# Performance work log

Hardware: AMD Instinct MI355X
Metric: run time of the kernel (lower is better)

## Reference

```python
import jax, jax.numpy as jnp
import numpy as np

# Fixed directional 3x3 stencils (order j=0..3 as in the torch module)
_K0 = [[0, 0, 0], [-0.5, 1, -0.5], [0, 0, 0]]
_K1 = [[0, 0, -0.5], [0, 1, 0], [-0.5, 0, 0]]
_K2 = [[0, -0.5, 0], [0, 1, 0], [0, -0.5, 0]]
_K3 = [[-0.5, 0, 0], [0, 1, 0], [0, 0, -0.5]]
KERNELS = jnp.asarray(np.stack([_K0, _K1, _K2, _K3])[:, None], dtype=jnp.float32)  # [4,1,3,3] OIHW
_EPS = 1e-5


def setup_inputs() -> dict:
    key = jax.random.key(0)
    x = jax.random.normal(key, (32, 3, 512, 512), dtype=jnp.float32)
    return {"x": x}


def reference(x):
    # grayscale: [B,1,H,W]
    gray = (0.3 * x[:, 0] + 0.59 * x[:, 1] + 0.11 * x[:, 2])[:, None]
    # one conv with 4 output channels instead of 4 separate 1-channel convs
    ltpe = jax.lax.conv_general_dilated(
        gray, KERNELS, window_strides=(1, 1), padding=((1, 1), (1, 1)),
        dimension_numbers=("NCHW", "OIHW", "NCHW"))  # [B,4,H,W]
    coeffs = (2.0 ** jnp.arange(4, dtype=jnp.float32)) / 15.0  # 2^j / 15
    # sum_j ((ltpe_j + 1) * 0.5) * coeff_j  -> [B,1,H,W]
    out = jnp.einsum("bjhw,j->bhw", (ltpe + 1.0) * 0.5, coeffs)[:, None]
    # InstanceNorm2d(1): per-(batch, channel) normalization over H,W, biased var, no affine
    mean = jnp.mean(out, axis=(2, 3), keepdims=True)
    var = jnp.var(out, axis=(2, 3), keepdims=True)
    out = (out - mean) * jax.lax.rsqrt(var + _EPS)
    return jnp.concatenate([out, out, out], axis=1)  # [B,3,H,W]
```

## Files before the change

kernel.cpp:

```cpp
#include <hip/hip_runtime.h>
#include <hip/hip_fp16.h>

#define IMGS 32
#define H 512
#define W 512
#define NPIX (H * W)
#define NTHR 256
#define RB 8
#define NBANDS (H / RB)
#define C4W (W / 4)

__device__ __forceinline__ float sten(float C, float L, float R, float U, float D,
                                      float UL, float UR, float DL, float DR) {
    const float c0 = 1.0f / 15.0f, c1 = 2.0f / 15.0f;
    const float c2 = 4.0f / 15.0f, c3 = 8.0f / 15.0f;
    const float acc = c0 * (L + R) + c1 * (UR + DL) + c2 * (U + D) + c3 * (UL + DR);
    return fmaf(-0.25f, acc, fmaf(0.5f, C, 0.5f));
}

template <typename ST>
__global__ __launch_bounds__(NTHR, 6) void k1_stencil(
    const float* __restrict__ x, ST* sout, size_t sstride,
    float2* __restrict__ partials)
{
    __shared__ float G[RB + 2][W];

    const int tid  = threadIdx.x;
    const int blk  = blockIdx.x;
    const int img  = blk >> 6;
    const int band = blk & (NBANDS - 1);
    const int r0   = band * RB;

    const float* xbase = x + (size_t)img * 3 * NPIX;
    ST* sbase = sout + (size_t)img * sstride;

#pragma unroll
    for (int it = 0; it < (RB + 2) * C4W / NTHR; ++it) {
        const int idx = it * NTHR + tid;
        const int ri  = idx >> 7;
        const int c4  = idx & (C4W - 1);
        const int gr  = r0 - 1 + ri;
        float4 g4 = make_float4(0.f, 0.f, 0.f, 0.f);
        if ((unsigned)gr < (unsigned)H) {
            const float* p = xbase + gr * W + c4 * 4;
            const float4 r = *(const float4*)p;
            const float4 g = *(const float4*)(p + NPIX);
            const float4 b = *(const float4*)(p + 2 * NPIX);
            g4.x = fmaf(0.3f, r.x, fmaf(0.59f, g.x, 0.11f * b.x));
            g4.y = fmaf(0.3f, r.y, fmaf(0.59f, g.y, 0.11f * b.y));
            g4.z = fmaf(0.3f, r.z, fmaf(0.59f, g.z, 0.11f * b.z));
            g4.w = fmaf(0.3f, r.w, fmaf(0.59f, g.w, 0.11f * b.w));
        }
        *(float4*)&G[ri][c4 * 4] = g4;
    }
    __syncthreads();

    const int c4   = tid & (C4W - 1);
    const int half = tid >> 7;
    const int lr0  = half * (RB / 2);

    float sum = 0.0f, sq = 0.0f;

    float4 a4 = *(const float4*)&G[lr0][c4 * 4];
    float4 b4 = *(const float4*)&G[lr0 + 1][c4 * 4];
    float aL = (c4 == 0) ? 0.0f : G[lr0][c4 * 4 - 1];
    float aR = (c4 == C4W - 1) ? 0.0f : G[lr0][c4 * 4 + 4];
    float bL = (c4 == 0) ? 0.0f : G[lr0 + 1][c4 * 4 - 1];
    float bR = (c4 == C4W - 1) ? 0.0f : G[lr0 + 1][c4 * 4 + 4];

#pragma unroll
    for (int k = 0; k < RB / 2; ++k) {
        const int lr = lr0 + k + 2;
        const float4 d4 = *(const float4*)&G[lr][c4 * 4];
        const float dL = (c4 == 0) ? 0.0f : G[lr][c4 * 4 - 1];
        const float dR = (c4 == C4W - 1) ? 0.0f : G[lr][c4 * 4 + 4];

        float4 o;
        o.x = sten(b4.x, bL,   b4.y, a4.x, d4.x, aL,   a4.y, dL,   d4.y);
        o.y = sten(b4.y, b4.x, b4.z, a4.y, d4.y, a4.x, a4.z, d4.x, d4.z);
        o.z = sten(b4.z, b4.y, b4.w, a4.z, d4.z, a4.y, a4.w, d4.y, d4.w);
        o.w = sten(b4.w, b4.z, bR,   a4.w, d4.w, a4.z, aR,   d4.z, dR);

        sum += (o.x + o.y) + (o.z + o.w);
        sq = fmaf(o.x, o.x, sq); sq = fmaf(o.y, o.y, sq);
        sq = fmaf(o.z, o.z, sq); sq = fmaf(o.w, o.w, sq);

        const size_t off = (size_t)(r0 + half * (RB / 2) + k) * W + c4 * 4;
        if constexpr (sizeof(ST) == 2) {
            union { __half h[4]; float2 f; } u;
            u.h[0] = __float2half_rn(o.x);
            u.h[1] = __float2half_rn(o.y);
            u.h[2] = __float2half_rn(o.z);
            u.h[3] = __float2half_rn(o.w);
            *(float2*)(sbase + off) = u.f;
        } else {
            *(float4*)(sbase + off) = o;
        }

        a4 = b4; aL = bL; aR = bR;
        b4 = d4; bL = dL; bR = dR;
    }

#pragma unroll
    for (int off = 32; off > 0; off >>= 1) {
        sum += __shfl_down(sum, off);
        sq  += __shfl_down(sq, off);
    }
    __syncthreads();
    const int wave = tid >> 6;
    const int lane = tid & 63;
    if (lane == 0) { G[0][wave] = sum; G[0][4 + wave] = sq; }
    __syncthreads();
    if (tid == 0) {
        partials[blk] = make_float2((G[0][0] + G[0][1]) + (G[0][2] + G[0][3]),
                                    (G[0][4] + G[0][5]) + (G[0][6] + G[0][7]));
    }
}

template <typename ST>
__global__ __launch_bounds__(NTHR) void k2_norm(
    const float2* __restrict__ partials, const ST* sin, size_t sstride,
    float* __restrict__ out)
{
    __shared__ float sm[2];

    const int tid = threadIdx.x;
    const int blk = blockIdx.x;
    const int img = blk >> 8;
    const int bi  = blk & 255;

    if (tid < 64) {
        const float2 p = partials[img * NBANDS + tid];
        float S1 = p.x, S2 = p.y;
#pragma unroll
        for (int off = 32; off > 0; off >>= 1) {
            S1 += __shfl_down(S1, off);
            S2 += __shfl_down(S2, off);
        }
        if (tid == 0) {
            const float m = S1 * (1.0f / NPIX);
            const float v = S2 * (1.0f / NPIX) - m * m;
            sm[0] = m;
            sm[1] = rsqrtf(v + 1e-5f);
        }
    }
    __syncthreads();
    const float mean = sm[0];
    const float rstd = sm[1];

    const ST* sb = sin + (size_t)img * sstride;
    float* base = out + (size_t)img * 3 * NPIX;
    const size_t off = (size_t)(bi * NTHR + tid) * 4;

    float4 v;
    if constexpr (sizeof(ST) == 2) {
        union { float2 f; __half h[4]; } u;
        u.f = *(const float2*)(sb + off);
        v.x = __half2float(u.h[0]); v.y = __half2float(u.h[1]);
        v.z = __half2float(u.h[2]); v.w = __half2float(u.h[3]);
    } else {
        v = *(const float4*)(sb + off);
    }
    v.x = (v.x - mean) * rstd;
    v.y = (v.y - mean) * rstd;
    v.z = (v.z - mean) * rstd;
    v.w = (v.w - mean) * rstd;
    *(float4*)(base + off) = v;
    *(float4*)(base + NPIX + off) = v;
    *(float4*)(base + 2 * NPIX + off) = v;
}

extern "C" void kernel_launch(void* const* d_in, const int* in_sizes, int n_in,
                              void* d_out, int out_size, void* d_ws, size_t ws_size,
                              hipStream_t stream) {
    const float* x = (const float*)d_in[0];
    float* out = (float*)d_out;

    const size_t s_bytes = (size_t)IMGS * NPIX * sizeof(__half);
    const size_t need = s_bytes + (size_t)IMGS * NBANDS * sizeof(float2);

    if (ws_size >= need) {
        __half* s = (__half*)d_ws;
        float2* partials = (float2*)((char*)d_ws + s_bytes);
        k1_stencil<__half><<<dim3(IMGS * NBANDS), dim3(NTHR), 0, stream>>>(
            x, s, (size_t)NPIX, partials);
        k2_norm<__half><<<dim3(IMGS * 256), dim3(NTHR), 0, stream>>>(
            partials, s, (size_t)NPIX, out);
    } else {
        float2* partials = (float2*)d_ws;
        k1_stencil<float><<<dim3(IMGS * NBANDS), dim3(NTHR), 0, stream>>>(
            x, out, (size_t)(3 * NPIX), partials);
        k2_norm<float><<<dim3(IMGS * 256), dim3(NTHR), 0, stream>>>(
            partials, out, (size_t)(3 * NPIX), out);
    }
}
```

Baseline: 45.75 us.

## Fuse stencil and instance norm into one pass with cross-block stat handoff

Merges the two kernels into a single launch. Each block keeps its stencil outputs in registers, publishes per-band partial sums, and the last block per image (found via an atomic counter) computes mean and rstd; every block spins until those stats are published and then writes the normalized output directly. This removes the intermediate half-precision buffer write and read and one kernel launch, and doubles rows per band to 16 so there are 1024 blocks. It depends on all 1024 blocks being co-resident, since blocks spin-wait on others; launch bounds allow 4 blocks per CU, and a memset is added each call.

```diff
diff --git a/kernel.cpp b/kernel.cpp
--- a/kernel.cpp
+++ b/kernel.cpp
@@ -1,14 +1,14 @@
 #include <hip/hip_runtime.h>
-#include <hip/hip_fp16.h>
 
 #define IMGS 32
 #define H 512
 #define W 512
 #define NPIX (H * W)
 #define NTHR 256
-#define RB 8
+#define RB 16
 #define NBANDS (H / RB)
 #define C4W (W / 4)
+#define NBLK (IMGS * NBANDS)
 
 __device__ __forceinline__ float sten(float C, float L, float R, float U, float D,
                                       float UL, float UR, float DL, float DR) {
@@ -18,21 +18,26 @@
     return fmaf(-0.25f, acc, fmaf(0.5f, C, 0.5f));
 }
 
-template <typename ST>
-__global__ __launch_bounds__(NTHR, 6) void k1_stencil(
-    const float* __restrict__ x, ST* sout, size_t sstride,
-    float2* __restrict__ partials)
+union PackF2 { float2 f; unsigned long long u; };
+
+__global__ __launch_bounds__(NTHR, 4) void ltpe_onepass(
+    const float* __restrict__ x, float* __restrict__ out,
+    unsigned long long* __restrict__ stats,
+    int* __restrict__ counters,
+    unsigned long long* __restrict__ partials)
 {
     __shared__ float G[RB + 2][W];
+    __shared__ float red[8];
+    __shared__ int fin;
+    __shared__ float sstat[2];
 
     const int tid  = threadIdx.x;
     const int blk  = blockIdx.x;
-    const int img  = blk >> 6;
+    const int img  = blk >> 5;
     const int band = blk & (NBANDS - 1);
     const int r0   = band * RB;
 
     const float* xbase = x + (size_t)img * 3 * NPIX;
-    ST* sbase = sout + (size_t)img * sstride;
 
 #pragma unroll
     for (int it = 0; it < (RB + 2) * C4W / NTHR; ++it) {
@@ -59,6 +64,7 @@
     const int half = tid >> 7;
     const int lr0  = half * (RB / 2);
 
+    float4 sreg[RB / 2];
     float sum = 0.0f, sq = 0.0f;
 
     float4 a4 = *(const float4*)&G[lr0][c4 * 4];
@@ -80,22 +86,11 @@
         o.y = sten(b4.y, b4.x, b4.z, a4.y, d4.y, a4.x, a4.z, d4.x, d4.z);
         o.z = sten(b4.z, b4.y, b4.w, a4.z, d4.z, a4.y, a4.w, d4.y, d4.w);
         o.w = sten(b4.w, b4.z, bR,   a4.w, d4.w, a4.z, aR,   d4.z, dR);
+        sreg[k] = o;
 
         sum += (o.x + o.y) + (o.z + o.w);
         sq = fmaf(o.x, o.x, sq); sq = fmaf(o.y, o.y, sq);
         sq = fmaf(o.z, o.z, sq); sq = fmaf(o.w, o.w, sq);
-
-        const size_t off = (size_t)(r0 + half * (RB / 2) + k) * W + c4 * 4;
-        if constexpr (sizeof(ST) == 2) {
-            union { __half h[4]; float2 f; } u;
-            u.h[0] = __float2half_rn(o.x);
-            u.h[1] = __float2half_rn(o.y);
-            u.h[2] = __float2half_rn(o.z);
-            u.h[3] = __float2half_rn(o.w);
-            *(float2*)(sbase + off) = u.f;
-        } else {
-            *(float4*)(sbase + off) = o;
-        }
 
         a4 = b4; aL = bL; aR = bR;
         b4 = d4; bL = dL; bR = dR;
@@ -106,32 +101,32 @@
         sum += __shfl_down(sum, off);
         sq  += __shfl_down(sq, off);
     }
-    __syncthreads();
     const int wave = tid >> 6;
     const int lane = tid & 63;
-    if (lane == 0) { G[0][wave] = sum; G[0][4 + wave] = sq; }
+    if (lane == 0) { red[wave] = sum; red[4 + wave] = sq; }
     __syncthreads();
+
     if (tid == 0) {
-        partials[blk] = make_float2((G[0][0] + G[0][1]) + (G[0][2] + G[0][3]),
-                                    (G[0][4] + G[0][5]) + (G[0][6] + G[0][7]));
+        PackF2 p;
+        p.f = make_float2((red[0] + red[1]) + (red[2] + red[3]),
+                          (red[4] + red[5]) + (red[6] + red[7]));
+        __hip_atomic_store(&partials[blk], p.u, __ATOMIC_RELEASE,
+                           __HIP_MEMORY_SCOPE_AGENT);
+        const int old = __hip_atomic_fetch_add(&counters[img], 1,
+                                               __ATOMIC_ACQ_REL,
+                                               __HIP_MEMORY_SCOPE_AGENT);
+        fin = (old == NBANDS - 1);
     }
-}
+    __syncthreads();
 
-template <typename ST>
-__global__ __launch_bounds__(NTHR) void k2_norm(
-    const float2* __restrict__ partials, const ST* sin, size_t sstride,
-    float* __restrict__ out)
-{
-    __shared__ float sm[2];
-
-    const int tid = threadIdx.x;
-    const int blk = blockIdx.x;
-    const int img = blk >> 8;
-    const int bi  = blk & 255;
-
-    if (tid < 64) {
-        const float2 p = partials[img * NBANDS + tid];
-        float S1 = p.x, S2 = p.y;
+    if (fin && tid < 64) {
+        float S1 = 0.0f, S2 = 0.0f;
+        if (tid < NBANDS) {
+            PackF2 p;
+            p.u = __hip_atomic_load(&partials[img * NBANDS + tid],
+                                    __ATOMIC_ACQUIRE, __HIP_MEMORY_SCOPE_AGENT);
+            S1 = p.f.x; S2 = p.f.y;
+        }
 #pragma unroll
         for (int off = 32; off > 0; off >>= 1) {
             S1 += __shfl_down(S1, off);
@@ -140,34 +135,41 @@
         if (tid == 0) {
             const float m = S1 * (1.0f / NPIX);
             const float v = S2 * (1.0f / NPIX) - m * m;
-            sm[0] = m;
-            sm[1] = rsqrtf(v + 1e-5f);
+            PackF2 st;
+            st.f = make_float2(m, rsqrtf(v + 1e-5f));
+            __hip_atomic_store(&stats[img], st.u, __ATOMIC_RELEASE,
+                               __HIP_MEMORY_SCOPE_AGENT);
         }
     }
+
+    if (tid == 0) {
+        PackF2 st;
+        for (;;) {
+            st.u = __hip_atomic_load(&stats[img], __ATOMIC_ACQUIRE,
+                                     __HIP_MEMORY_SCOPE_AGENT);
+            if (st.u != 0ULL) break;
+            __builtin_amdgcn_s_sleep(2);
+        }
+        sstat[0] = st.f.x;
+        sstat[1] = st.f.y;
+    }
     __syncthreads();
-    const float mean = sm[0];
-    const float rstd = sm[1];
+    const float mean = sstat[0];
+    const float rstd = sstat[1];
 
-    const ST* sb = sin + (size_t)img * sstride;
-    float* base = out + (size_t)img * 3 * NPIX;
-    const size_t off = (size_t)(bi * NTHR + tid) * 4;
-
-    float4 v;
-    if constexpr (sizeof(ST) == 2) {
-        union { float2 f; __half h[4]; } u;
-        u.f = *(const float2*)(sb + off);
-        v.x = __half2float(u.h[0]); v.y = __half2float(u.h[1]);
-        v.z = __half2float(u.h[2]); v.w = __half2float(u.h[3]);
-    } else {
-        v = *(const float4*)(sb + off);
+    float* obase = out + (size_t)img * 3 * NPIX;
+#pragma unroll
+    for (int k = 0; k < RB / 2; ++k) {
+        float4 o = sreg[k];
+        o.x = (o.x - mean) * rstd;
+        o.y = (o.y - mean) * rstd;
+        o.z = (o.z - mean) * rstd;
+        o.w = (o.w - mean) * rstd;
+        const size_t off = (size_t)(r0 + half * (RB / 2) + k) * W + c4 * 4;
+        *(float4*)(obase + off) = o;
+        *(float4*)(obase + NPIX + off) = o;
+        *(float4*)(obase + 2 * NPIX + off) = o;
     }
-    v.x = (v.x - mean) * rstd;
-    v.y = (v.y - mean) * rstd;
-    v.z = (v.z - mean) * rstd;
-    v.w = (v.w - mean) * rstd;
-    *(float4*)(base + off) = v;
-    *(float4*)(base + NPIX + off) = v;
-    *(float4*)(base + 2 * NPIX + off) = v;
 }
 
 extern "C" void kernel_launch(void* const* d_in, const int* in_sizes, int n_in,
@@ -176,21 +178,12 @@
     const float* x = (const float*)d_in[0];
     float* out = (float*)d_out;
 
-    const size_t s_bytes = (size_t)IMGS * NPIX * sizeof(__half);
-    const size_t need = s_bytes + (size_t)IMGS * NBANDS * sizeof(float2);
+    unsigned long long* stats = (unsigned long long*)d_ws;
+    int* counters = (int*)((char*)d_ws + 256);
+    unsigned long long* partials = (unsigned long long*)((char*)d_ws + 512);
 
-    if (ws_size >= need) {
-        __half* s = (__half*)d_ws;
-        float2* partials = (float2*)((char*)d_ws + s_bytes);
-        k1_stencil<__half><<<dim3(IMGS * NBANDS), dim3(NTHR), 0, stream>>>(
-            x, s, (size_t)NPIX, partials);
-        k2_norm<__half><<<dim3(IMGS * 256), dim3(NTHR), 0, stream>>>(
-            partials, s, (size_t)NPIX, out);
-    } else {
-        float2* partials = (float2*)d_ws;
-        k1_stencil<float><<<dim3(IMGS * NBANDS), dim3(NTHR), 0, stream>>>(
-            x, out, (size_t)(3 * NPIX), partials);
-        k2_norm<float><<<dim3(IMGS * 256), dim3(NTHR), 0, stream>>>(
-            partials, out, (size_t)(3 * NPIX), out);
-    }
+    hipMemsetAsync(d_ws, 0, 512, stream);
+
+    ltpe_onepass<<<dim3(NBLK), dim3(NTHR), 0, stream>>>(
+        x, out, stats, counters, partials);
 }
```

Result: slower. 113.6 us (+148.4%).

## Recompute stencil in normalize pass instead of staging fp16 intermediate

Applied to the files above, without the earlier changes.

The first kernel now only computes per-band sum and sum-of-squares, and the second kernel recomputes grayscale and stencil from x, normalizes, and writes the output directly. This removes the fp16 intermediate write and read and its half-precision rounding. The second kernel visits bands in reverse order so recently read input may still be in the last-level cache, and it uses nontemporal stores for the output. The trade-off is reading the input twice and doing the stencil arithmetic twice.

```diff
diff --git a/kernel.cpp b/kernel.cpp
--- a/kernel.cpp
+++ b/kernel.cpp
@@ -1,5 +1,4 @@
 #include <hip/hip_runtime.h>
-#include <hip/hip_fp16.h>
 
 #define IMGS 32
 #define H 512
@@ -9,6 +8,9 @@
 #define RB 8
 #define NBANDS (H / RB)
 #define C4W (W / 4)
+#define NBLK (IMGS * NBANDS)
+
+typedef float vfloat4 __attribute__((ext_vector_type(4)));
 
 __device__ __forceinline__ float sten(float C, float L, float R, float U, float D,
                                       float UL, float UR, float DL, float DR) {
@@ -18,22 +20,8 @@
     return fmaf(-0.25f, acc, fmaf(0.5f, C, 0.5f));
 }
 
-template <typename ST>
-__global__ __launch_bounds__(NTHR, 6) void k1_stencil(
-    const float* __restrict__ x, ST* sout, size_t sstride,
-    float2* __restrict__ partials)
-{
-    __shared__ float G[RB + 2][W];
-
-    const int tid  = threadIdx.x;
-    const int blk  = blockIdx.x;
-    const int img  = blk >> 6;
-    const int band = blk & (NBANDS - 1);
-    const int r0   = band * RB;
-
-    const float* xbase = x + (size_t)img * 3 * NPIX;
-    ST* sbase = sout + (size_t)img * sstride;
-
+__device__ __forceinline__ void stage_gray(const float* __restrict__ xbase,
+                                           int r0, int tid, float G[RB + 2][W]) {
 #pragma unroll
     for (int it = 0; it < (RB + 2) * C4W / NTHR; ++it) {
         const int idx = it * NTHR + tid;
@@ -53,6 +41,21 @@
         }
         *(float4*)&G[ri][c4 * 4] = g4;
     }
+}
+
+__global__ __launch_bounds__(NTHR) void k1_stats(
+    const float* __restrict__ x, float2* __restrict__ partials)
+{
+    __shared__ float G[RB + 2][W];
+    __shared__ float red[8];
+
+    const int tid  = threadIdx.x;
+    const int blk  = blockIdx.x;
+    const int img  = blk >> 6;
+    const int band = blk & (NBANDS - 1);
+    const int r0   = band * RB;
+
+    stage_gray(x + (size_t)img * 3 * NPIX, r0, tid, G);
     __syncthreads();
 
     const int c4   = tid & (C4W - 1);
@@ -85,18 +88,6 @@
         sq = fmaf(o.x, o.x, sq); sq = fmaf(o.y, o.y, sq);
         sq = fmaf(o.z, o.z, sq); sq = fmaf(o.w, o.w, sq);
 
-        const size_t off = (size_t)(r0 + half * (RB / 2) + k) * W + c4 * 4;
-        if constexpr (sizeof(ST) == 2) {
-            union { __half h[4]; float2 f; } u;
-            u.h[0] = __float2half_rn(o.x);
-            u.h[1] = __float2half_rn(o.y);
-            u.h[2] = __float2half_rn(o.z);
-            u.h[3] = __float2half_rn(o.w);
-            *(float2*)(sbase + off) = u.f;
-        } else {
-            *(float4*)(sbase + off) = o;
-        }
-
         a4 = b4; aL = bL; aR = bR;
         b4 = d4; bL = dL; bR = dR;
     }
@@ -106,28 +97,30 @@
         sum += __shfl_down(sum, off);
         sq  += __shfl_down(sq, off);
     }
-    __syncthreads();
     const int wave = tid >> 6;
     const int lane = tid & 63;
-    if (lane == 0) { G[0][wave] = sum; G[0][4 + wave] = sq; }
+    if (lane == 0) { red[wave] = sum; red[4 + wave] = sq; }
     __syncthreads();
     if (tid == 0) {
-        partials[blk] = make_float2((G[0][0] + G[0][1]) + (G[0][2] + G[0][3]),
-                                    (G[0][4] + G[0][5]) + (G[0][6] + G[0][7]));
+        partials[blk] = make_float2((red[0] + red[1]) + (red[2] + red[3]),
+                                    (red[4] + red[5]) + (red[6] + red[7]));
     }
 }
 
-template <typename ST>
 __global__ __launch_bounds__(NTHR) void k2_norm(
-    const float2* __restrict__ partials, const ST* sin, size_t sstride,
+    const float* __restrict__ x, const float2* __restrict__ partials,
     float* __restrict__ out)
 {
+    __shared__ float G[RB + 2][W];
     __shared__ float sm[2];
 
     const int tid = threadIdx.x;
-    const int blk = blockIdx.x;
-    const int img = blk >> 8;
-    const int bi  = blk & 255;
+    const int b   = blockIdx.x;
+    const int g   = b >> 3;
+    const int blk = (((NBLK / 8 - 1) - g) << 3) | (b & 7);
+    const int img  = blk >> 6;
+    const int band = blk & (NBANDS - 1);
+    const int r0   = band * RB;
 
     if (tid < 64) {
         const float2 p = partials[img * NBANDS + tid];
@@ -144,30 +137,53 @@
             sm[1] = rsqrtf(v + 1e-5f);
         }
     }
+
+    stage_gray(x + (size_t)img * 3 * NPIX, r0, tid, G);
     __syncthreads();
+
     const float mean = sm[0];
     const float rstd = sm[1];
 
-    const ST* sb = sin + (size_t)img * sstride;
-    float* base = out + (size_t)img * 3 * NPIX;
-    const size_t off = (size_t)(bi * NTHR + tid) * 4;
+    const int c4   = tid & (C4W - 1);
+    const int half = tid >> 7;
+    const int lr0  = half * (RB / 2);
 
-    float4 v;
-    if constexpr (sizeof(ST) == 2) {
-        union { float2 f; __half h[4]; } u;
-        u.f = *(const float2*)(sb + off);
-        v.x = __half2float(u.h[0]); v.y = __half2float(u.h[1]);
-        v.z = __half2float(u.h[2]); v.w = __half2float(u.h[3]);
-    } else {
-        v = *(const float4*)(sb + off);
+    float* obase = out + (size_t)img * 3 * NPIX;
+
+    float4 a4 = *(const float4*)&G[lr0][c4 * 4];
+    float4 b4 = *(const float4*)&G[lr0 + 1][c4 * 4];
+    float aL = (c4 == 0) ? 0.0f : G[lr0][c4 * 4 - 1];
+    float aR = (c4 == C4W - 1) ? 0.0f : G[lr0][c4 * 4 + 4];
+    float bL = (c4 == 0) ? 0.0f : G[lr0 + 1][c4 * 4 - 1];
+    float bR = (c4 == C4W - 1) ? 0.0f : G[lr0 + 1][c4 * 4 + 4];
+
+#pragma unroll
+    for (int k = 0; k < RB / 2; ++k) {
+        const int lr = lr0 + k + 2;
+        const float4 d4 = *(const float4*)&G[lr][c4 * 4];
+        const float dL = (c4 == 0) ? 0.0f : G[lr][c4 * 4 - 1];
+        const float dR = (c4 == C4W - 1) ? 0.0f : G[lr][c4 * 4 + 4];
+
+        float4 o;
+        o.x = sten(b4.x, bL,   b4.y, a4.x, d4.x, aL,   a4.y, dL,   d4.y);
+        o.y = sten(b4.y, b4.x, b4.z, a4.y, d4.y, a4.x, a4.z, d4.x, d4.z);
+        o.z = sten(b4.z, b4.y, b4.w, a4.z, d4.z, a4.y, a4.w, d4.y, d4.w);
+        o.w = sten(b4.w, b4.z, bR,   a4.w, d4.w, a4.z, aR,   d4.z, dR);
+
+        vfloat4 v;
+        v.x = (o.x - mean) * rstd;
+        v.y = (o.y - mean) * rstd;
+        v.z = (o.z - mean) * rstd;
+        v.w = (o.w - mean) * rstd;
+
+        const size_t off = (size_t)(r0 + half * (RB / 2) + k) * W + c4 * 4;
+        __builtin_nontemporal_store(v, (vfloat4*)(obase + off));
+        __builtin_nontemporal_store(v, (vfloat4*)(obase + NPIX + off));
+        __builtin_nontemporal_store(v, (vfloat4*)(obase + 2 * NPIX + off));
+
+        a4 = b4; aL = bL; aR = bR;
+        b4 = d4; bL = dL; bR = dR;
     }
-    v.x = (v.x - mean) * rstd;
-    v.y = (v.y - mean) * rstd;
-    v.z = (v.z - mean) * rstd;
-    v.w = (v.w - mean) * rstd;
-    *(float4*)(base + off) = v;
-    *(float4*)(base + NPIX + off) = v;
-    *(float4*)(base + 2 * NPIX + off) = v;
 }
 
 extern "C" void kernel_launch(void* const* d_in, const int* in_sizes, int n_in,
@@ -175,22 +191,8 @@
                               hipStream_t stream) {
     const float* x = (const float*)d_in[0];
     float* out = (float*)d_out;
+    float2* partials = (float2*)d_ws;
 
-    const size_t s_bytes = (size_t)IMGS * NPIX * sizeof(__half);
-    const size_t need = s_bytes + (size_t)IMGS * NBANDS * sizeof(float2);
-
-    if (ws_size >= need) {
-        __half* s = (__half*)d_ws;
-        float2* partials = (float2*)((char*)d_ws + s_bytes);
-        k1_stencil<__half><<<dim3(IMGS * NBANDS), dim3(NTHR), 0, stream>>>(
-            x, s, (size_t)NPIX, partials);
-        k2_norm<__half><<<dim3(IMGS * 256), dim3(NTHR), 0, stream>>>(
-            partials, s, (size_t)NPIX, out);
-    } else {
-        float2* partials = (float2*)d_ws;
-        k1_stencil<float><<<dim3(IMGS * NBANDS), dim3(NTHR), 0, stream>>>(
-            x, out, (size_t)(3 * NPIX), partials);
-        k2_norm<float><<<dim3(IMGS * 256), dim3(NTHR), 0, stream>>>(
-            partials, out, (size_t)(3 * NPIX), out);
-    }
+    k1_stats<<<dim3(NBLK), dim3(NTHR), 0, stream>>>(x, partials);
+    k2_norm<<<dim3(NBLK), dim3(NTHR), 0, stream>>>(x, partials, out);
 }
```

Result: slower. 57.59 us (+25.9%).
